# Performance work log

Measured on AMD Instinct MI355X. Metric: run time of the kernel, lower is better.

## Reference

```python
import jax, jax.numpy as jnp
import numpy as np

B, S, D = 1, 2048, 4096
H, KVH, HD = 32, 8, 128
WIN = 2048
REPEATS = H // KVH
SCALE = HD ** -0.5
NEG = -1e9


def setup_inputs() -> dict:
    key = jax.random.key(0)
    ks = jax.random.split(key, 5)
    x = jax.random.normal(ks[0], (B, S, D), dtype=jnp.float32) * 0.02
    wq = jax.random.normal(ks[1], (H * HD, D), dtype=jnp.float32) * (D ** -0.5)
    wk = jax.random.normal(ks[2], (KVH * HD, D), dtype=jnp.float32) * (D ** -0.5)
    wv = jax.random.normal(ks[3], (KVH * HD, D), dtype=jnp.float32) * (D ** -0.5)
    wo = jax.random.normal(ks[4], (H * HD, D), dtype=jnp.float32).T * ((H * HD) ** -0.5)
    wo = jnp.asarray(wo)  # [D, H*HD] torch-style (out, in) = (D, H*HD)
    positions = jnp.arange(S, dtype=jnp.int32)
    # rotary tables: freqs_cis[s, j] = exp(i * s * theta_j), theta_j = 10000^(-2j/HD)
    theta = 10000.0 ** (-jnp.arange(0, HD, 2, dtype=jnp.float32) / HD)  # [HD/2]
    ang = positions[:, None].astype(jnp.float32) * theta[None, :]       # [S, HD/2]
    freqs_cos = jnp.cos(ang)
    freqs_sin = jnp.sin(ang)
    # sliding-window causal additive mask [S, S]
    i = jnp.arange(S)[:, None]
    j = jnp.arange(S)[None, :]
    allowed = (j <= i) & (i - j < WIN)
    mask = jnp.where(allowed, 0.0, NEG).astype(jnp.float32)
    return {"x": x, "freqs_cos": freqs_cos, "freqs_sin": freqs_sin,
            "wq": wq, "wk": wk, "wv": wv, "wo": wo,
            "mask": mask, "positions": positions}


def _apply_rope(t, cos, sin):
    # t: [B, S, h, HD]; pairs are (even, odd) interleaved -> complex mul
    tr = t[..., 0::2]  # real parts [B,S,h,HD/2]
    ti = t[..., 1::2]  # imag parts
    c = cos[None, :, None, :]
    s = sin[None, :, None, :]
    out_r = tr * c - ti * s
    out_i = tr * s + ti * c
    return jnp.stack([out_r, out_i], axis=-1).reshape(t.shape)


def reference(x, freqs_cos, freqs_sin, wq, wk, wv, wo, mask, positions):
    bsz, seqlen, _ = x.shape
    q = (x @ wq.T).reshape(bsz, seqlen, H, HD)
    k = (x @ wk.T).reshape(bsz, seqlen, KVH, HD)
    v = (x @ wv.T).reshape(bsz, seqlen, KVH, HD)
    q = _apply_rope(q, freqs_cos, freqs_sin)
    k = _apply_rope(k, freqs_cos, freqs_sin)
    # GQA: repeat_interleave kv heads to match query heads (prefill path)
    k = jnp.repeat(k, REPEATS, axis=2)  # [B,S,H,HD]
    v = jnp.repeat(v, REPEATS, axis=2)
    scores = jnp.einsum("bqhd,bkhd->bhqk", q, k) * SCALE
    scores = scores + mask[None, None, :, :]
    probs = jax.nn.softmax(scores, axis=-1)
    out = jnp.einsum("bhqk,bkhd->bqhd", probs, v)
    out = out.reshape(bsz, seqlen, H * HD)
    return out @ wo.T
```

## Files before the change

kernel.cpp:

```cpp
#include <hip/hip_runtime.h>
#include <hip/hip_bf16.h>
#include <stdint.h>

#define SEQ    2048
#define DMODEL 4096
#define NH     32
#define NKVH   8
#define HDIM   128
#define KVD    (NKVH*HDIM)
#define QD     (NH*HDIM)
#define QKVN   (QD + 2*KVD)
#define ASCALE 0.08838834764831845f

typedef __attribute__((ext_vector_type(8))) short s8v;
typedef __attribute__((ext_vector_type(4))) short s4v;
typedef __attribute__((ext_vector_type(4))) float f4v;

#define MFMA16(acc, a, b) \
  asm("v_mfma_f32_16x16x32_bf16 %0, %1, %2, %0" : "+v"(acc) : "v"(a), "v"(b))

#define SBAR() do { __builtin_amdgcn_sched_barrier(0); \
                    __builtin_amdgcn_s_barrier();      \
                    __builtin_amdgcn_sched_barrier(0); } while (0)

__device__ __forceinline__ void gl2lds16(const void* g, void* l) {
  __builtin_amdgcn_global_load_lds(
      (const __attribute__((address_space(1))) void*)g,
      (__attribute__((address_space(3))) void*)l, 16, 0, 0);
}

__global__ __launch_bounds__(256) void k_cvt5(const float* __restrict__ x,
                                              const float* __restrict__ wq,
                                              const float* __restrict__ wk,
                                              const float* __restrict__ wv,
                                              const float* __restrict__ wo,
                                              __hip_bfloat16* __restrict__ xb,
                                              __hip_bfloat16* __restrict__ wf,
                                              __hip_bfloat16* __restrict__ wob) {
  int i = blockIdx.x * 256 + threadIdx.x;
  const float* src;
  __hip_bfloat16* dst;
  float scale = 1.0f;
  if (i < 1048576)       { src = x;  dst = xb; }
  else if (i < 3145728)  { src = wq; dst = wf;  i -= 1048576; scale = ASCALE; }
  else if (i < 3670016)  { src = wk; dst = wf + (size_t)QD * DMODEL;  i -= 3145728; }
  else if (i < 4194304)  { src = wv; dst = wf + (size_t)(QD + KVD) * DMODEL; i -= 3670016; }
  else                   { src = wo; dst = wob; i -= 4194304; }
  const float4* p = (const float4*)src + (size_t)i * 2;
  float4 a = p[0], b = p[1];
  union { __hip_bfloat16 h[8]; s8v v; } o;
  o.h[0] = __float2bfloat16(a.x * scale); o.h[1] = __float2bfloat16(a.y * scale);
  o.h[2] = __float2bfloat16(a.z * scale); o.h[3] = __float2bfloat16(a.w * scale);
  o.h[4] = __float2bfloat16(b.x * scale); o.h[5] = __float2bfloat16(b.y * scale);
  o.h[6] = __float2bfloat16(b.z * scale); o.h[7] = __float2bfloat16(b.w * scale);
  *(s8v*)(dst + (size_t)i * 8) = o.v;
}

__global__ __launch_bounds__(256) void k_rope(__hip_bfloat16* __restrict__ t,
                                              const float* __restrict__ fc,
                                              const float* __restrict__ fs, int heads) {
  int pid = blockIdx.x * 256 + threadIdx.x;
  int i = pid & 63;
  int rest = pid >> 6;
  int h = rest % heads;
  int s = rest / heads;
  size_t base = ((size_t)s * heads + h) * HDIM + 2 * i;
  uint32_t u = *(const uint32_t*)(t + base);
  __hip_bfloat16 hh[2]; *(uint32_t*)hh = u;
  float tr = __bfloat162float(hh[0]), ti = __bfloat162float(hh[1]);
  float c = fc[(size_t)s * 64 + i], sv = fs[(size_t)s * 64 + i];
  hh[0] = __float2bfloat16(tr * c - ti * sv);
  hh[1] = __float2bfloat16(tr * sv + ti * c);
  *(uint32_t*)(t + base) = *(uint32_t*)hh;
}

__global__ __launch_bounds__(512, 2) void k_qkv(const __hip_bfloat16* __restrict__ A,
                                                const __hip_bfloat16* __restrict__ W,
                                                __hip_bfloat16* __restrict__ Qb,
                                                __hip_bfloat16* __restrict__ Kc,
                                                __hip_bfloat16* __restrict__ Vt) {
  __shared__ __align__(16) __hip_bfloat16 sm[2][256 * 64 + 192 * 64];
  const int t5 = threadIdx.x;
  const int wave = t5 >> 6, lane = t5 & 63;
  const int lrow = lane & 15, kq = lane >> 4;
  const int wm = wave >> 2, wn = wave & 3;
  const int mt = blockIdx.x & 7, nt = blockIdx.x >> 3;
  const int m0 = mt * 256, n0 = nt * 192;

  auto stageA = [&](int p, int kt) {
#pragma unroll
    for (int it = 0; it < 4; ++it) {
      int chunk = it * 512 + t5;
      int r = chunk >> 3, cc = ((chunk & 7) ^ (r & 7)) * 8;
      gl2lds16(A + (size_t)(m0 + r) * DMODEL + kt * 64 + cc,
               (char*)&sm[p][0] + it * 8192 + wave * 1024);
    }
  };
  auto stageB = [&](int p, int kt) {
#pragma unroll
    for (int it = 0; it < 3; ++it) {
      int chunk = it * 512 + t5;
      int r = chunk >> 3, cc = ((chunk & 7) ^ (r & 7)) * 8;
      gl2lds16(W + (size_t)(n0 + r) * DMODEL + kt * 64 + cc,
               (char*)&sm[p][0] + 32768 + it * 8192 + wave * 1024);
    }
  };

  f4v acc[8][3] = {};

  stageA(0, 0); stageB(0, 0);
  stageA(1, 1); stageB(1, 1);

  const int NT = DMODEL / 64;
#pragma unroll 2
  for (int t = 0; t < NT; ++t) {
    const int p = t & 1;
    const __hip_bfloat16* As = &sm[p][0];
    const __hip_bfloat16* Bs = &sm[p][256 * 64];

    __builtin_amdgcn_sched_barrier(0);
    if (t == NT - 1) asm volatile("s_waitcnt vmcnt(0)" ::: "memory");
    else             asm volatile("s_waitcnt vmcnt(7)" ::: "memory");
    __builtin_amdgcn_s_barrier();
    __builtin_amdgcn_sched_barrier(0);

    s8v a0[8], b0[3];
#pragma unroll
    for (int m = 0; m < 8; ++m) {
      int row = wm * 128 + m * 16 + lrow;
      a0[m] = *(const s8v*)&As[row * 64 + ((kq * 8) ^ ((row & 7) << 3))];
    }
#pragma unroll
    for (int n = 0; n < 3; ++n) {
      int row = wn * 48 + n * 16 + lrow;
      b0[n] = *(const s8v*)&Bs[row * 64 + ((kq * 8) ^ ((row & 7) << 3))];
    }
    __builtin_amdgcn_s_setprio(1);
#pragma unroll
    for (int m = 0; m < 4; ++m)
#pragma unroll
      for (int n = 0; n < 3; ++n) MFMA16(acc[m][n], a0[m], b0[n]);
    __builtin_amdgcn_s_setprio(0);
    SBAR();

    s8v a1[8], b1[3];
#pragma unroll
    for (int m = 0; m < 8; ++m) {
      int row = wm * 128 + m * 16 + lrow;
      a1[m] = *(const s8v*)&As[row * 64 + ((32 + kq * 8) ^ ((row & 7) << 3))];
    }
#pragma unroll
    for (int n = 0; n < 3; ++n) {
      int row = wn * 48 + n * 16 + lrow;
      b1[n] = *(const s8v*)&Bs[row * 64 + ((32 + kq * 8) ^ ((row & 7) << 3))];
    }
    __builtin_amdgcn_s_setprio(1);
#pragma unroll
    for (int m = 4; m < 8; ++m)
#pragma unroll
      for (int n = 0; n < 3; ++n) MFMA16(acc[m][n], a0[m], b0[n]);
    __builtin_amdgcn_s_setprio(0);
    SBAR();

    if (t + 2 < NT) stageA(p, t + 2);
    __builtin_amdgcn_s_setprio(1);
#pragma unroll
    for (int m = 0; m < 4; ++m)
#pragma unroll
      for (int n = 0; n < 3; ++n) MFMA16(acc[m][n], a1[m], b1[n]);
    __builtin_amdgcn_s_setprio(0);
    SBAR();

    if (t + 2 < NT) stageB(p, t + 2);
    __builtin_amdgcn_s_setprio(1);
#pragma unroll
    for (int m = 4; m < 8; ++m)
#pragma unroll
      for (int n = 0; n < 3; ++n) MFMA16(acc[m][n], a1[m], b1[n]);
    __builtin_amdgcn_s_setprio(0);
  }

#pragma unroll
  for (int m = 0; m < 8; ++m)
#pragma unroll
    for (int n = 0; n < 3; ++n) {
      int c = n0 + wn * 48 + n * 16 + lrow;
      int r0 = m0 + wm * 128 + m * 16 + kq * 4;
      if (c < QD) {
#pragma unroll
        for (int j = 0; j < 4; ++j)
          Qb[(size_t)(r0 + j) * QD + c] = __float2bfloat16(acc[m][n][j]);
      } else if (c < QD + KVD) {
#pragma unroll
        for (int j = 0; j < 4; ++j)
          Kc[(size_t)(r0 + j) * KVD + (c - QD)] = __float2bfloat16(acc[m][n][j]);
      } else {
        union { __hip_bfloat16 b[4]; s4v v; } u;
#pragma unroll
        for (int j = 0; j < 4; ++j) u.b[j] = __float2bfloat16(acc[m][n][j]);
        *(s4v*)&Vt[(size_t)(c - QD - KVD) * SEQ + r0] = u.v;
      }
    }
}

__global__ __launch_bounds__(512, 2) void k_oproj(const __hip_bfloat16* __restrict__ A,
                                                  const __hip_bfloat16* __restrict__ B,
                                                  float* __restrict__ C) {
  __shared__ __align__(16) __hip_bfloat16 sm[2][128 * 64 + 256 * 64];
  const int t5 = threadIdx.x;
  const int wave = t5 >> 6, lane = t5 & 63;
  const int lrow = lane & 15, kq = lane >> 4;
  const int wm = wave >> 2, wn = wave & 3;
  const int m0 = blockIdx.y * 128, n0 = blockIdx.x * 256;

  auto stageA = [&](int p, int kt) {
#pragma unroll
    for (int it = 0; it < 2; ++it) {
      int chunk = it * 512 + t5;
      int r = chunk >> 3, cc = ((chunk & 7) ^ (r & 7)) * 8;
      gl2lds16(A + (size_t)(m0 + r) * QD + kt * 64 + cc,
               (char*)&sm[p][0] + it * 8192 + wave * 1024);
    }
  };
  auto stageB = [&](int p, int kt) {
#pragma unroll
    for (int it = 0; it < 4; ++it) {
      int chunk = it * 512 + t5;
      int r = chunk >> 3, cc = ((chunk & 7) ^ (r & 7)) * 8;
      gl2lds16(B + (size_t)(n0 + r) * QD + kt * 64 + cc,
               (char*)&sm[p][0] + 16384 + it * 8192 + wave * 1024);
    }
  };

  f4v acc[4][4] = {};

  stageA(0, 0); stageB(0, 0);
  stageA(1, 1); stageB(1, 1);

  const int NT = QD / 64;
#pragma unroll 2
  for (int t = 0; t < NT; ++t) {
    const int p = t & 1;
    const __hip_bfloat16* As = &sm[p][0];
    const __hip_bfloat16* Bs = &sm[p][128 * 64];

    __builtin_amdgcn_sched_barrier(0);
    if (t == NT - 1) asm volatile("s_waitcnt vmcnt(0)" ::: "memory");
    else             asm volatile("s_waitcnt vmcnt(6)" ::: "memory");
    __builtin_amdgcn_s_barrier();
    __builtin_amdgcn_sched_barrier(0);

    s8v a0[4], b0[4];
#pragma unroll
    for (int m = 0; m < 4; ++m) {
      int row = wm * 64 + m * 16 + lrow;
      a0[m] = *(const s8v*)&As[row * 64 + ((kq * 8) ^ ((row & 7) << 3))];
    }
#pragma unroll
    for (int n = 0; n < 4; ++n) {
      int row = wn * 64 + n * 16 + lrow;
      b0[n] = *(const s8v*)&Bs[row * 64 + ((kq * 8) ^ ((row & 7) << 3))];
    }
    __builtin_amdgcn_s_setprio(1);
#pragma unroll
    for (int m = 0; m < 2; ++m)
#pragma unroll
      for (int n = 0; n < 4; ++n) MFMA16(acc[m][n], a0[m], b0[n]);
    __builtin_amdgcn_s_setprio(0);
    SBAR();

    s8v a1[4], b1[4];
#pragma unroll
    for (int m = 0; m < 4; ++m) {
      int row = wm * 64 + m * 16 + lrow;
      a1[m] = *(const s8v*)&As[row * 64 + ((32 + kq * 8) ^ ((row & 7) << 3))];
    }
#pragma unroll
    for (int n = 0; n < 4; ++n) {
      int row = wn * 64 + n * 16 + lrow;
      b1[n] = *(const s8v*)&Bs[row * 64 + ((32 + kq * 8) ^ ((row & 7) << 3))];
    }
    __builtin_amdgcn_s_setprio(1);
#pragma unroll
    for (int m = 2; m < 4; ++m)
#pragma unroll
      for (int n = 0; n < 4; ++n) MFMA16(acc[m][n], a0[m], b0[n]);
    __builtin_amdgcn_s_setprio(0);
    SBAR();

    if (t + 2 < NT) stageA(p, t + 2);
    __builtin_amdgcn_s_setprio(1);
#pragma unroll
    for (int m = 0; m < 2; ++m)
#pragma unroll
      for (int n = 0; n < 4; ++n) MFMA16(acc[m][n], a1[m], b1[n]);
    __builtin_amdgcn_s_setprio(0);
    SBAR();

    if (t + 2 < NT) stageB(p, t + 2);
    __builtin_amdgcn_s_setprio(1);
#pragma unroll
    for (int m = 2; m < 4; ++m)
#pragma unroll
      for (int n = 0; n < 4; ++n) MFMA16(acc[m][n], a1[m], b1[n]);
    __builtin_amdgcn_s_setprio(0);
  }

#pragma unroll
  for (int m = 0; m < 4; ++m)
#pragma unroll
    for (int n = 0; n < 4; ++n)
#pragma unroll
      for (int j = 0; j < 4; ++j) {
        int r = m0 + wm * 64 + m * 16 + kq * 4 + j;
        int c = n0 + wn * 64 + n * 16 + lrow;
        C[(size_t)r * DMODEL + c] = acc[m][n][j];
      }
}

__global__ __launch_bounds__(256, 2) void k_flash(const __hip_bfloat16* __restrict__ Q,
                                                  const __hip_bfloat16* __restrict__ Kb,
                                                  const __hip_bfloat16* __restrict__ Vtg,
                                                  __hip_bfloat16* __restrict__ O) {
  __shared__ __align__(16) __hip_bfloat16 Ks[2][64 * 128];
  __shared__ __align__(16) __hip_bfloat16 Vs[144 * 64];
  __shared__ __align__(16) __hip_bfloat16 Ps[4][16 * 64];
  const int qp = blockIdx.x, h = blockIdx.y, g = h >> 2;
  const int t = threadIdx.x, wave = t >> 6, lane = t & 63;
  const int lrow = lane & 15, kq = lane >> 4;
  const int qtA = qp, qtB = 31 - qp;

  s8v qfA[4], qfB[4];
  {
    const int qrA = qtA * 64 + wave * 16 + lrow;
    const int qrB = qtB * 64 + wave * 16 + lrow;
#pragma unroll
    for (int tt = 0; tt < 4; ++tt) {
      qfA[tt] = *(const s8v*)(Q + (size_t)qrA * QD + h * HDIM + tt * 32 + kq * 8);
      qfB[tt] = *(const s8v*)(Q + (size_t)qrB * QD + h * HDIM + tt * 32 + kq * 8);
    }
  }

  if (t < 128) {
    union { __hip_bfloat16 h8[8]; s8v v; } one;
#pragma unroll
    for (int e = 0; e < 8; ++e) one.h8[e] = __float2bfloat16(1.0f);
    *(s8v*)&Vs[128 * 64 + t * 8] = one.v;
  }

  f4v oA[9] = {}, oB[9] = {};
  float mA = -1e30f, mB = -1e30f;

  auto stage_k = [&](int buf, int kv) {
#pragma unroll
    for (int it = 0; it < 4; ++it) {
      int chunk = it * 256 + t;
      int r = chunk >> 4, cc = ((chunk & 15) ^ (r & 7)) * 8;
      gl2lds16(Kb + (size_t)(kv * 64 + r) * KVD + g * HDIM + cc,
               (char*)&Ks[buf][0] + it * 4096 + wave * 1024);
    }
  };
  auto stage_v = [&](int kv) {
#pragma unroll
    for (int it = 0; it < 4; ++it) {
      int chunk = it * 256 + t;
      int d = chunk >> 3, cc = ((chunk & 7) ^ (d & 7)) * 8;
      gl2lds16(Vtg + (size_t)(g * HDIM + d) * SEQ + kv * 64 + cc,
               (char*)Vs + it * 4096 + wave * 1024);
    }
  };

  auto soft_pv = [&](f4v (&s)[4], int qt, int kv, f4v (&acc_o)[9], float& mrun) {
    __hip_bfloat16* P = &Ps[wave][0];
    const bool diag = (kv == qt);
    const int qi = qt * 64 + wave * 16 + lrow;
    const int swz = (lrow & 7) << 3;
    float pv[4][4];
    float mx = -1e30f;
#pragma unroll
    for (int n = 0; n < 4; ++n)
#pragma unroll
      for (int j = 0; j < 4; ++j) {
        float v = s[n][j];
        if (diag) {
          int ki = kv * 64 + n * 16 + kq * 4 + j;
          if (ki > qi) v = -1e30f;
        }
        pv[n][j] = v;
        mx = fmaxf(mx, v);
      }
    mx = fmaxf(mx, __shfl_xor(mx, 16, 64));
    mx = fmaxf(mx, __shfl_xor(mx, 32, 64));
    if (!__all(mx <= mrun)) {
      float mnew = fmaxf(mrun, mx);
      float fsc = __expf(mrun - mnew);
      mrun = mnew;
      float fj[4];
#pragma unroll
      for (int j = 0; j < 4; ++j) fj[j] = __shfl(fsc, kq * 4 + j, 64);
#pragma unroll
      for (int n = 0; n < 9; ++n) {
        acc_o[n][0] *= fj[0]; acc_o[n][1] *= fj[1];
        acc_o[n][2] *= fj[2]; acc_o[n][3] *= fj[3];
      }
    }
    asm volatile("" ::: "memory");
#pragma unroll
    for (int n = 0; n < 4; ++n) {
      union { __hip_bfloat16 b[4]; s4v v; } u;
#pragma unroll
      for (int j = 0; j < 4; ++j) u.b[j] = __float2bfloat16(__expf(pv[n][j] - mrun));
      *(s4v*)&P[lrow * 64 + ((n * 16 + kq * 4) ^ swz)] = u.v;
    }
    asm volatile("" ::: "memory");
#pragma unroll
    for (int tt = 0; tt < 2; ++tt) {
      s8v pa = *(const s8v*)&P[lrow * 64 + ((tt * 32 + kq * 8) ^ swz)];
#pragma unroll
      for (int n = 0; n < 9; ++n) {
        int d = n * 16 + lrow;
        s8v vf = *(const s8v*)&Vs[d * 64 + ((tt * 32 + kq * 8) ^ ((d & 7) << 3))];
        MFMA16(acc_o[n], pa, vf);
      }
    }
  };

  stage_k(0, 0);
  int cur = 0;
  for (int kv = 0; kv <= qtB; ++kv) {
    const bool actA = (kv <= qtA);
    __syncthreads();
    if (kv < qtB) stage_k(cur ^ 1, kv + 1);
    stage_v(kv);

    f4v sB[4] = {}, sA[4] = {};
    if (actA) {
#pragma unroll
      for (int tt = 0; tt < 4; ++tt)
#pragma unroll
        for (int n = 0; n < 4; ++n) {
          int row = n * 16 + lrow;
          s8v kf = *(const s8v*)&Ks[cur][row * 128 + ((tt * 32 + kq * 8) ^ ((row & 7) << 3))];
          MFMA16(sB[n], kf, qfB[tt]);
          MFMA16(sA[n], kf, qfA[tt]);
        }
    } else {
#pragma unroll
      for (int tt = 0; tt < 4; ++tt)
#pragma unroll
        for (int n = 0; n < 4; ++n) {
          int row = n * 16 + lrow;
          s8v kf = *(const s8v*)&Ks[cur][row * 128 + ((tt * 32 + kq * 8) ^ ((row & 7) << 3))];
          MFMA16(sB[n], kf, qfB[tt]);
        }
    }
    __syncthreads();

    soft_pv(sB, qtB, kv, oB, mB);
    if (actA) soft_pv(sA, qtA, kv, oA, mA);
    cur ^= 1;
  }

#pragma unroll
  for (int n = 0; n < 8; ++n)
#pragma unroll
    for (int j = 0; j < 4; ++j) {
      int d = n * 16 + lrow;
      int qiB = qtB * 64 + wave * 16 + kq * 4 + j;
      O[(size_t)qiB * QD + h * HDIM + d] = __float2bfloat16(oB[n][j] / oB[8][j]);
      int qiA = qtA * 64 + wave * 16 + kq * 4 + j;
      O[(size_t)qiA * QD + h * HDIM + d] = __float2bfloat16(oA[n][j] / oA[8][j]);
    }
}

extern "C" void kernel_launch(void* const* d_in, const int* in_sizes, int n_in,
                              void* d_out, int out_size, void* d_ws, size_t ws_size,
                              hipStream_t stream) {
  const float* x  = (const float*)d_in[0];
  const float* fc = (const float*)d_in[1];
  const float* fs = (const float*)d_in[2];
  const float* wq = (const float*)d_in[3];
  const float* wk = (const float*)d_in[4];
  const float* wv = (const float*)d_in[5];
  const float* wo = (const float*)d_in[6];
  float* out = (float*)d_out;

  char* ws = (char*)d_ws;
  auto alloc = [&](size_t bytes) {
    char* p = ws;
    ws += (bytes + 255) & ~(size_t)255;
    return p;
  };
  __hip_bfloat16* xb  = (__hip_bfloat16*)alloc((size_t)SEQ * DMODEL * 2);
  __hip_bfloat16* wf  = (__hip_bfloat16*)alloc((size_t)QKVN * DMODEL * 2);
  __hip_bfloat16* wob = (__hip_bfloat16*)alloc((size_t)DMODEL * QD * 2);
  __hip_bfloat16* Qb  = (__hip_bfloat16*)alloc((size_t)SEQ * QD * 2);
  __hip_bfloat16* Kc  = (__hip_bfloat16*)alloc((size_t)SEQ * KVD * 2);
  __hip_bfloat16* Vtg = (__hip_bfloat16*)alloc((size_t)KVD * SEQ * 2);
  __hip_bfloat16* Ob  = (__hip_bfloat16*)alloc((size_t)SEQ * QD * 2);

  k_cvt5<<<dim3(24576), dim3(256), 0, stream>>>(x, wq, wk, wv, wo, xb, wf, wob);

  k_qkv<<<dim3(256), dim3(512), 0, stream>>>(xb, wf, Qb, Kc, Vtg);

  k_rope<<<dim3(SEQ * NH * 64 / 256), 256, 0, stream>>>(Qb, fc, fs, NH);
  k_rope<<<dim3(SEQ * NKVH * 64 / 256), 256, 0, stream>>>(Kc, fc, fs, NKVH);

  k_flash<<<dim3(16, NH), 256, 0, stream>>>(Qb, Kc, Vtg, Ob);

  k_oproj<<<dim3(DMODEL / 256, SEQ / 128), dim3(512), 0, stream>>>(Ob, wob, out);
}
```

Before: 277.5 us.

## Reshape QKV GEMM wave tiling and compute softmax row sums explicitly in flash

The QKV projection GEMM changes its wave layout from 2x4 to 4x2, so each wave now computes a 64x96 tile instead of 128x48. This changes the ratio of LDS fragment loads to MFMAs per wave. In the flash kernel, the ninth 'ones' column of V, used to accumulate the softmax denominator via MFMA, is dropped. The row sum is now computed with scalar adds plus cross-lane shuffles, which removes two MFMAs and two LDS reads per k-step per query tile at the cost of extra VALU and shuffle work.

```diff
diff --git a/kernel.cpp b/kernel.cpp
--- a/kernel.cpp
+++ b/kernel.cpp
@@ -83,7 +83,7 @@
   const int t5 = threadIdx.x;
   const int wave = t5 >> 6, lane = t5 & 63;
   const int lrow = lane & 15, kq = lane >> 4;
-  const int wm = wave >> 2, wn = wave & 3;
+  const int wm = wave >> 1, wn = wave & 1;
   const int mt = blockIdx.x & 7, nt = blockIdx.x >> 3;
   const int m0 = mt * 256, n0 = nt * 192;
 
@@ -106,7 +106,7 @@
     }
   };
 
-  f4v acc[8][3] = {};
+  f4v acc[4][6] = {};
 
   stageA(0, 0); stageB(0, 0);
   stageA(1, 1); stageB(1, 1);
@@ -124,68 +124,68 @@
     __builtin_amdgcn_s_barrier();
     __builtin_amdgcn_sched_barrier(0);
 
-    s8v a0[8], b0[3];
-#pragma unroll
-    for (int m = 0; m < 8; ++m) {
-      int row = wm * 128 + m * 16 + lrow;
+    s8v a0[4], b0[6];
+#pragma unroll
+    for (int m = 0; m < 4; ++m) {
+      int row = wm * 64 + m * 16 + lrow;
       a0[m] = *(const s8v*)&As[row * 64 + ((kq * 8) ^ ((row & 7) << 3))];
     }
 #pragma unroll
-    for (int n = 0; n < 3; ++n) {
-      int row = wn * 48 + n * 16 + lrow;
+    for (int n = 0; n < 6; ++n) {
+      int row = wn * 96 + n * 16 + lrow;
       b0[n] = *(const s8v*)&Bs[row * 64 + ((kq * 8) ^ ((row & 7) << 3))];
     }
     __builtin_amdgcn_s_setprio(1);
 #pragma unroll
-    for (int m = 0; m < 4; ++m)
-#pragma unroll
-      for (int n = 0; n < 3; ++n) MFMA16(acc[m][n], a0[m], b0[n]);
+    for (int m = 0; m < 2; ++m)
+#pragma unroll
+      for (int n = 0; n < 6; ++n) MFMA16(acc[m][n], a0[m], b0[n]);
     __builtin_amdgcn_s_setprio(0);
     SBAR();
 
-    s8v a1[8], b1[3];
-#pragma unroll
-    for (int m = 0; m < 8; ++m) {
-      int row = wm * 128 + m * 16 + lrow;
+    s8v a1[4], b1[6];
+#pragma unroll
+    for (int m = 0; m < 4; ++m) {
+      int row = wm * 64 + m * 16 + lrow;
       a1[m] = *(const s8v*)&As[row * 64 + ((32 + kq * 8) ^ ((row & 7) << 3))];
     }
 #pragma unroll
-    for (int n = 0; n < 3; ++n) {
-      int row = wn * 48 + n * 16 + lrow;
+    for (int n = 0; n < 6; ++n) {
+      int row = wn * 96 + n * 16 + lrow;
       b1[n] = *(const s8v*)&Bs[row * 64 + ((32 + kq * 8) ^ ((row & 7) << 3))];
     }
     __builtin_amdgcn_s_setprio(1);
 #pragma unroll
-    for (int m = 4; m < 8; ++m)
-#pragma unroll
-      for (int n = 0; n < 3; ++n) MFMA16(acc[m][n], a0[m], b0[n]);
+    for (int m = 2; m < 4; ++m)
+#pragma unroll
+      for (int n = 0; n < 6; ++n) MFMA16(acc[m][n], a0[m], b0[n]);
     __builtin_amdgcn_s_setprio(0);
     SBAR();
 
     if (t + 2 < NT) stageA(p, t + 2);
     __builtin_amdgcn_s_setprio(1);
 #pragma unroll
-    for (int m = 0; m < 4; ++m)
-#pragma unroll
-      for (int n = 0; n < 3; ++n) MFMA16(acc[m][n], a1[m], b1[n]);
+    for (int m = 0; m < 2; ++m)
+#pragma unroll
+      for (int n = 0; n < 6; ++n) MFMA16(acc[m][n], a1[m], b1[n]);
     __builtin_amdgcn_s_setprio(0);
     SBAR();
 
     if (t + 2 < NT) stageB(p, t + 2);
     __builtin_amdgcn_s_setprio(1);
 #pragma unroll
-    for (int m = 4; m < 8; ++m)
-#pragma unroll
-      for (int n = 0; n < 3; ++n) MFMA16(acc[m][n], a1[m], b1[n]);
+    for (int m = 2; m < 4; ++m)
+#pragma unroll
+      for (int n = 0; n < 6; ++n) MFMA16(acc[m][n], a1[m], b1[n]);
     __builtin_amdgcn_s_setprio(0);
   }
 
 #pragma unroll
-  for (int m = 0; m < 8; ++m)
-#pragma unroll
-    for (int n = 0; n < 3; ++n) {
-      int c = n0 + wn * 48 + n * 16 + lrow;
-      int r0 = m0 + wm * 128 + m * 16 + kq * 4;
+  for (int m = 0; m < 4; ++m)
+#pragma unroll
+    for (int n = 0; n < 6; ++n) {
+      int c = n0 + wn * 96 + n * 16 + lrow;
+      int r0 = m0 + wm * 64 + m * 16 + kq * 4;
       if (c < QD) {
 #pragma unroll
         for (int j = 0; j < 4; ++j)
@@ -323,7 +323,7 @@
                                                   const __hip_bfloat16* __restrict__ Vtg,
                                                   __hip_bfloat16* __restrict__ O) {
   __shared__ __align__(16) __hip_bfloat16 Ks[2][64 * 128];
-  __shared__ __align__(16) __hip_bfloat16 Vs[144 * 64];
+  __shared__ __align__(16) __hip_bfloat16 Vs[128 * 64];
   __shared__ __align__(16) __hip_bfloat16 Ps[4][16 * 64];
   const int qp = blockIdx.x, h = blockIdx.y, g = h >> 2;
   const int t = threadIdx.x, wave = t >> 6, lane = t & 63;
@@ -341,15 +341,9 @@
     }
   }
 
-  if (t < 128) {
-    union { __hip_bfloat16 h8[8]; s8v v; } one;
-#pragma unroll
-    for (int e = 0; e < 8; ++e) one.h8[e] = __float2bfloat16(1.0f);
-    *(s8v*)&Vs[128 * 64 + t * 8] = one.v;
-  }
-
-  f4v oA[9] = {}, oB[9] = {};
+  f4v oA[8] = {}, oB[8] = {};
   float mA = -1e30f, mB = -1e30f;
+  float lA = 0.f, lB = 0.f;
 
   auto stage_k = [&](int buf, int kv) {
 #pragma unroll
@@ -370,7 +364,7 @@
     }
   };
 
-  auto soft_pv = [&](f4v (&s)[4], int qt, int kv, f4v (&acc_o)[9], float& mrun) {
+  auto soft_pv = [&](f4v (&s)[4], int qt, int kv, f4v (&acc_o)[8], float& mrun, float& lrun) {
     __hip_bfloat16* P = &Ps[wave][0];
     const bool diag = (kv == qt);
     const int qi = qt * 64 + wave * 16 + lrow;
@@ -395,29 +389,38 @@
       float mnew = fmaxf(mrun, mx);
       float fsc = __expf(mrun - mnew);
       mrun = mnew;
+      lrun *= fsc;
       float fj[4];
 #pragma unroll
       for (int j = 0; j < 4; ++j) fj[j] = __shfl(fsc, kq * 4 + j, 64);
 #pragma unroll
-      for (int n = 0; n < 9; ++n) {
+      for (int n = 0; n < 8; ++n) {
         acc_o[n][0] *= fj[0]; acc_o[n][1] *= fj[1];
         acc_o[n][2] *= fj[2]; acc_o[n][3] *= fj[3];
       }
     }
+    float rsum = 0.f;
     asm volatile("" ::: "memory");
 #pragma unroll
     for (int n = 0; n < 4; ++n) {
       union { __hip_bfloat16 b[4]; s4v v; } u;
 #pragma unroll
-      for (int j = 0; j < 4; ++j) u.b[j] = __float2bfloat16(__expf(pv[n][j] - mrun));
+      for (int j = 0; j < 4; ++j) {
+        __hip_bfloat16 pb = __float2bfloat16(__expf(pv[n][j] - mrun));
+        u.b[j] = pb;
+        rsum += __bfloat162float(pb);
+      }
       *(s4v*)&P[lrow * 64 + ((n * 16 + kq * 4) ^ swz)] = u.v;
     }
+    rsum += __shfl_xor(rsum, 16, 64);
+    rsum += __shfl_xor(rsum, 32, 64);
+    lrun += rsum;
     asm volatile("" ::: "memory");
 #pragma unroll
     for (int tt = 0; tt < 2; ++tt) {
       s8v pa = *(const s8v*)&P[lrow * 64 + ((tt * 32 + kq * 8) ^ swz)];
 #pragma unroll
-      for (int n = 0; n < 9; ++n) {
+      for (int n = 0; n < 8; ++n) {
         int d = n * 16 + lrow;
         s8v vf = *(const s8v*)&Vs[d * 64 + ((tt * 32 + kq * 8) ^ ((d & 7) << 3))];
         MFMA16(acc_o[n], pa, vf);
@@ -456,20 +459,26 @@
     }
     __syncthreads();
 
-    soft_pv(sB, qtB, kv, oB, mB);
-    if (actA) soft_pv(sA, qtA, kv, oA, mA);
+    soft_pv(sB, qtB, kv, oB, mB, lB);
+    if (actA) soft_pv(sA, qtA, kv, oA, mA, lA);
     cur ^= 1;
   }
 
+  float ljB[4], ljA[4];
+#pragma unroll
+  for (int j = 0; j < 4; ++j) {
+    ljB[j] = __shfl(lB, kq * 4 + j, 64);
+    ljA[j] = __shfl(lA, kq * 4 + j, 64);
+  }
 #pragma unroll
   for (int n = 0; n < 8; ++n)
 #pragma unroll
     for (int j = 0; j < 4; ++j) {
       int d = n * 16 + lrow;
       int qiB = qtB * 64 + wave * 16 + kq * 4 + j;
-      O[(size_t)qiB * QD + h * HDIM + d] = __float2bfloat16(oB[n][j] / oB[8][j]);
+      O[(size_t)qiB * QD + h * HDIM + d] = __float2bfloat16(oB[n][j] / ljB[j]);
       int qiA = qtA * 64 + wave * 16 + kq * 4 + j;
-      O[(size_t)qiA * QD + h * HDIM + d] = __float2bfloat16(oA[n][j] / oA[8][j]);
+      O[(size_t)qiA * QD + h * HDIM + d] = __float2bfloat16(oA[n][j] / ljA[j]);
     }
 }
 
```

Result: no change. 280.5 us (+1.1%).
